# Kernel optimization log

Measured on AMD Instinct MI355X. Metric: run time of the kernel, lower is better.

Reference implementation:

```python
import jax, jax.numpy as jnp
import numpy as np
from jax import lax

N = 8388608
NG = 1024
TAU = 0.1
GAMMA = 0.05
MAX_ITERS = 30
EPS = 1e-9


def setup_inputs() -> dict:
    key = jax.random.key(0)
    k1, k2, k3 = jax.random.split(key, 3)
    y_raw = jax.random.uniform(k1, (N,), dtype=jnp.float32)
    y_real = jax.random.uniform(k2, (N,), dtype=jnp.float32)
    group_ids = jax.random.randint(k3, (N,), 0, NG, dtype=jnp.int32)
    return {"y_raw": y_raw, "y_real": y_real, "group_ids": group_ids, "n_groups": NG}


def reference(y_raw, y_real, group_ids, n_groups):
    y_real = jnp.maximum(y_real, EPS)
    l = (1.0 - TAU) * y_real          # per-element lower box bound
    u = (1.0 + TAU) * y_real          # per-element upper box bound
    y_clipped = jnp.clip(y_raw, l, u)
    w = 1.0 / jnp.maximum(y_real, 1e-9)

    seg_sum = lambda v: jax.ops.segment_sum(v, group_ids, num_segments=n_groups)

    n_g = seg_sum(jnp.ones_like(y_raw))            # [G] group sizes
    L = (1.0 - GAMMA) * n_g
    U = (1.0 + GAMMA) * n_g
    S0 = seg_sum(w * y_clipped)                    # [G] ratio sums at alpha=0
    feasible = (S0 >= L) & (S0 <= U)

    # per-group bracketing interval for alpha
    alo = jax.ops.segment_min((l - y_raw) * w, group_ids, num_segments=n_groups) - 1.0
    ahi = jax.ops.segment_max((u - y_raw) * w, group_ids, num_segments=n_groups) + 1.0
    nonempty = n_g > 0
    alo = jnp.where(nonempty, alo, 0.0)            # guard empty groups (inf/-inf)
    ahi = jnp.where(nonempty, ahi, 0.0)
    T = jnp.where(S0 < L, L, U)                    # [G] bisection target

    def step(carry, _):
        lo, hi, _ = carry
        mid = 0.5 * (lo + hi)                                    # [G]
        y_mid = jnp.clip(y_raw + mid[group_ids] / w, l, u)       # [N]
        Smid = seg_sum(w * y_mid)                                # [G]
        lo = jnp.where(Smid < T, mid, lo)
        hi = jnp.where(Smid >= T, mid, hi)
        return (lo, hi, mid), None

    (lo, hi, mid), _ = lax.scan(step, (alo, ahi, alo), None, length=MAX_ITERS)
    y_bis = jnp.clip(y_raw + mid[group_ids] / w, l, u)           # last iterate y_mid
    return jnp.where(feasible[group_ids], y_clipped, y_bis)
```

## Files before the change

### kernel.cpp

```cpp
#include <hip/hip_runtime.h>

#define NGROUPS  1024
#define EPSF     1e-9f
#define MAX_ITERS 30
#define SUM_MASK ((1ull << 49) - 1)
#define CNT_SHIFT 49
#define FIX_SCALE 1073741824.0f
#define FIX_INV   (1.0 / 1073741824.0)

__device__ __forceinline__ unsigned enc_f(float f) {
    unsigned u = __float_as_uint(f);
    return (u & 0x80000000u) ? ~u : (u | 0x80000000u);
}
__device__ __forceinline__ float dec_f(unsigned e) {
    unsigned u = (e & 0x80000000u) ? (e ^ 0x80000000u) : ~e;
    return __uint_as_float(u);
}

__global__ __launch_bounds__(NGROUPS) void k_init(unsigned long long* gpack,
                                                  unsigned* gmn, unsigned* gmx) {
    int g = threadIdx.x;
    gpack[g] = 0ull;
    gmn[g]   = 0xFFFFFFFFu;
    gmx[g]   = 0u;
}

__global__ __launch_bounds__(1024) void k_stats(const float4* __restrict__ yraw4,
                                                const float4* __restrict__ yreal4,
                                                const int4*   __restrict__ gid4,
                                                float4*       __restrict__ out4,
                                                unsigned long long* gpack, int n4) {
    __shared__ unsigned long long s_pk[NGROUPS];
    int t = threadIdx.x;
    s_pk[t] = 0ull;
    __syncthreads();

    int base = blockIdx.x * 4096;
    float4 yr[4], ye[4];
    int4   gg[4];
    bool   ok[4];
#pragma unroll
    for (int k = 0; k < 4; ++k) {
        int i = base + k * 1024 + t;
        ok[k] = (i < n4);
        if (ok[k]) { yr[k] = yraw4[i]; ye[k] = yreal4[i]; gg[k] = gid4[i]; }
    }
#pragma unroll
    for (int k = 0; k < 4; ++k) {
        if (!ok[k]) continue;
        float yrs[4] = { yr[k].x, yr[k].y, yr[k].z, yr[k].w };
        float yes[4] = { ye[k].x, ye[k].y, ye[k].z, ye[k].w };
        int   gs[4]  = { gg[k].x, gg[k].y, gg[k].z, gg[k].w };
        float oc[4];
#pragma unroll
        for (int j = 0; j < 4; ++j) {
            float yraw = yrs[j];
            float yrc  = fmaxf(yes[j], EPSF);
            float l = 0.9f * yrc;
            float u = 1.1f * yrc;
            float yclip = fminf(fmaxf(yraw, l), u);
            oc[j] = yclip;
            float s = yclip / yrc;
            unsigned long long pk = (1ull << CNT_SHIFT)
                + (unsigned long long)__float2uint_rn(s * FIX_SCALE);
            atomicAdd(&s_pk[gs[j]], pk);
        }
        out4[base + k * 1024 + t] = make_float4(oc[0], oc[1], oc[2], oc[3]);
    }
    __syncthreads();
    if (s_pk[t] != 0ull) atomicAdd(&gpack[t], s_pk[t]);
}

__global__ __launch_bounds__(NGROUPS) void k_group(const unsigned long long* gpack,
                                                   unsigned* feas, float* gT,
                                                   float* galpha, unsigned* gbase,
                                                   unsigned* gcur, unsigned* total) {
    __shared__ unsigned s_scan[NGROUPS];
    int g = threadIdx.x;
    unsigned long long pk = gpack[g];
    unsigned c = (unsigned)(pk >> CNT_SHIFT);
    float S0 = (float)((double)(pk & SUM_MASK) * FIX_INV);
    float n  = (float)c;
    float L = 0.95f * n;
    float U = 1.05f * n;
    unsigned f = (S0 >= L && S0 <= U) ? 1u : 0u;
    feas[g]   = f;
    gT[g]     = (S0 < L) ? L : U;
    galpha[g] = 0.0f;

    unsigned v = f ? 0u : c;
    s_scan[g] = v;
    for (int off = 1; off < NGROUPS; off <<= 1) {
        __syncthreads();
        unsigned tmp = (g >= off) ? s_scan[g - off] : 0u;
        __syncthreads();
        s_scan[g] += tmp;
    }
    __syncthreads();
    unsigned incl = s_scan[g];
    unsigned base = incl - v;
    gbase[g] = base;
    gcur[g]  = base;
    if (g == NGROUPS - 1) *total = incl;
}

__global__ __launch_bounds__(256) void k_mmc(const float4* __restrict__ yraw4,
                                             const float4* __restrict__ yreal4,
                                             const int4*   __restrict__ gid4,
                                             const unsigned* __restrict__ feas,
                                             unsigned* gcur, const unsigned* total,
                                             unsigned* gmn, unsigned* gmx,
                                             unsigned* cidx, unsigned* cgid,
                                             unsigned capacity, int n4) {
    if (*total == 0u) return;
    __shared__ unsigned s_feas[NGROUPS];
    __shared__ unsigned s_mn[NGROUPS];
    __shared__ unsigned s_mx[NGROUPS];
    for (int g = threadIdx.x; g < NGROUPS; g += blockDim.x) {
        s_feas[g] = feas[g]; s_mn[g] = 0xFFFFFFFFu; s_mx[g] = 0u;
    }
    __syncthreads();
    int stride = gridDim.x * blockDim.x;
    for (int i = blockIdx.x * blockDim.x + threadIdx.x; i < n4; i += stride) {
        int4 gg = gid4[i];
        int gs[4] = { gg.x, gg.y, gg.z, gg.w };
        bool any = !s_feas[gs[0]] || !s_feas[gs[1]] || !s_feas[gs[2]] || !s_feas[gs[3]];
        if (!any) continue;
        float4 yr = yraw4[i];
        float4 ye = yreal4[i];
        float yrs[4] = { yr.x, yr.y, yr.z, yr.w };
        float yes[4] = { ye.x, ye.y, ye.z, ye.w };
#pragma unroll
        for (int j = 0; j < 4; ++j) {
            int g = gs[j];
            if (s_feas[g]) continue;
            float yraw = yrs[j];
            float yrc  = fmaxf(yes[j], EPSF);
            float l = 0.9f * yrc;
            float u = 1.1f * yrc;
            float w = 1.0f / yrc;
            float a0 = (l - yraw) * w;
            float a1 = (u - yraw) * w;
            atomicMin(&s_mn[g], enc_f(a0));
            atomicMax(&s_mx[g], enc_f(a1));
            unsigned pos = atomicAdd(&gcur[g], 1u);
            if (pos < capacity) {
                cidx[pos] = (unsigned)(4 * i + j);
                cgid[pos] = (unsigned)g;
            }
        }
    }
    __syncthreads();
    for (int g = threadIdx.x; g < NGROUPS; g += blockDim.x) {
        if (!s_feas[g]) {
            atomicMin(&gmn[g], s_mn[g]);
            atomicMax(&gmx[g], s_mx[g]);
        }
    }
}

#define CAPC 8064
__global__ __launch_bounds__(256) void k_bisect(const float* __restrict__ y_raw,
                                                const float* __restrict__ y_real,
                                                const unsigned* feas,
                                                const unsigned long long* gpack,
                                                const unsigned* gbase, const float* gT,
                                                const unsigned* gmn, const unsigned* gmx,
                                                float* galpha,
                                                const unsigned* __restrict__ cidx,
                                                unsigned capacity) {
    int g = blockIdx.x;
    if (feas[g]) return;
    __shared__ float2 cache[CAPC];
    __shared__ double s_part[4];
    __shared__ float  s_mid;
    unsigned base = gbase[g];
    unsigned cnt  = (unsigned)(gpack[g] >> CNT_SHIFT);
    if (base >= capacity) cnt = 0;
    else if (cnt > capacity - base) cnt = capacity - base;
    int t = threadIdx.x;
    for (unsigned i = t; i < cnt && i < CAPC; i += 256u) {
        unsigned idx = cidx[base + i];
        cache[i] = make_float2(y_raw[idx], y_real[idx]);
    }
    __syncthreads();
    float lo = dec_f(gmn[g]) - 1.0f;
    float hi = dec_f(gmx[g]) + 1.0f;
    float T  = gT[g];
    float mid = lo;
    for (int it = 0; it < MAX_ITERS; ++it) {
        if (t == 0) s_mid = 0.5f * (lo + hi);
        __syncthreads();
        float m = s_mid;
        double part = 0.0;
        for (unsigned i = t; i < cnt; i += 256u) {
            float yraw, ye;
            if (i < CAPC) { float2 v = cache[i]; yraw = v.x; ye = v.y; }
            else { unsigned idx = cidx[base + i]; yraw = y_raw[idx]; ye = y_real[idx]; }
            float yrc = fmaxf(ye, EPSF);
            float l = 0.9f * yrc;
            float u = 1.1f * yrc;
            float w = 1.0f / yrc;
            float ym = fminf(fmaxf(yraw + m / w, l), u);
            part += (double)(w * ym);
        }
#pragma unroll
        for (int off = 32; off > 0; off >>= 1) part += __shfl_down(part, off, 64);
        if ((t & 63) == 0) s_part[t >> 6] = part;
        __syncthreads();
        if (t == 0) {
            float Smid = (float)(s_part[0] + s_part[1] + s_part[2] + s_part[3]);
            if (Smid < T) lo = m; else hi = m;
        }
        mid = m;
        __syncthreads();
    }
    if (t == 0) galpha[g] = mid;
}

__global__ __launch_bounds__(256) void k_fixup(const float* __restrict__ y_raw,
                                               const float* __restrict__ y_real,
                                               const unsigned* __restrict__ cidx,
                                               const unsigned* __restrict__ cgid,
                                               const float* galpha, const unsigned* total,
                                               float* __restrict__ out, unsigned capacity) {
    unsigned tot = *total;
    if (tot > capacity) tot = capacity;
    unsigned stride = gridDim.x * blockDim.x;
    for (unsigned i = blockIdx.x * blockDim.x + threadIdx.x; i < tot; i += stride) {
        unsigned idx = cidx[i];
        unsigned g   = cgid[i];
        float yraw = y_raw[idx];
        float yrc  = fmaxf(y_real[idx], EPSF);
        float l = 0.9f * yrc;
        float u = 1.1f * yrc;
        float w = 1.0f / yrc;
        float a = galpha[g];
        out[idx] = fminf(fmaxf(yraw + a / w, l), u);
    }
}

extern "C" void kernel_launch(void* const* d_in, const int* in_sizes, int n_in,
                              void* d_out, int out_size, void* d_ws, size_t ws_size,
                              hipStream_t stream) {
    const float* y_raw  = (const float*)d_in[0];
    const float* y_real = (const float*)d_in[1];
    const int*   gid    = (const int*)d_in[2];
    float* out = (float*)d_out;
    const int n  = in_sizes[0];
    const int n4 = n / 4;

    char* ws = (char*)d_ws;
    unsigned long long* gpack = (unsigned long long*)(ws + 0);
    unsigned* gmn    = (unsigned*)(ws + 8192);
    unsigned* gmx    = (unsigned*)(ws + 12288);
    unsigned* feas   = (unsigned*)(ws + 16384);
    float*    gT     = (float*)(ws + 20480);
    float*    galpha = (float*)(ws + 24576);
    unsigned* gbase  = (unsigned*)(ws + 28672);
    unsigned* gcur   = (unsigned*)(ws + 32768);
    unsigned* total  = (unsigned*)(ws + 36864);
    unsigned* cidx   = (unsigned*)(ws + 40960);
    size_t cap64 = (ws_size > 40960) ? (ws_size - 40960) / 8 : 0;
    if (cap64 > (size_t)n) cap64 = (size_t)n;
    unsigned capacity = (unsigned)cap64;
    unsigned* cgid = cidx + capacity;

    int nb_stats = (n4 + 4095) / 4096;

    k_init<<<1, NGROUPS, 0, stream>>>(gpack, gmn, gmx);
    k_stats<<<nb_stats, 1024, 0, stream>>>((const float4*)y_raw, (const float4*)y_real,
                                           (const int4*)gid, (float4*)out, gpack, n4);
    k_group<<<1, NGROUPS, 0, stream>>>(gpack, feas, gT, galpha, gbase, gcur, total);
    k_mmc<<<512, 256, 0, stream>>>((const float4*)y_raw, (const float4*)y_real,
                                   (const int4*)gid, feas, gcur, total,
                                   gmn, gmx, cidx, cgid, capacity, n4);
    k_bisect<<<NGROUPS, 256, 0, stream>>>(y_raw, y_real, feas, gpack, gbase, gT,
                                          gmn, gmx, galpha, cidx, capacity);
    k_fixup<<<512, 256, 0, stream>>>(y_raw, y_real, cidx, cgid, galpha, total,
                                     out, capacity);
}
```

Measured before the change: 150.7 us.

## Fuse group finalize into stats via last-block and fixup into bisection

Merges the per-group feasibility and prefix-scan kernel into the stats kernel, using a last-block-done counter with a threadfence. Bisection blocks now write the final clipped outputs for their own group, so the separate fixup kernel goes away. Stats switches to 512-thread blocks, adds an exact-tiling variant without bounds checks, and uses nontemporal output stores. The aim is to remove two launches and their serialization gaps, at the cost of a serial tail in the last block and a dependence on the done counter being reset each call.

Measured after the change: 410.3 us. +172.3%, slower.

```diff
diff --git a/kernel.cpp b/kernel.cpp
--- a/kernel.cpp
+++ b/kernel.cpp
@@ -7,6 +7,10 @@
 #define CNT_SHIFT 49
 #define FIX_SCALE 1073741824.0f
 #define FIX_INV   (1.0 / 1073741824.0)
+#define SBLK 512
+#define STILE 4
+
+typedef float vfloat4 __attribute__((ext_vector_type(4)));
 
 __device__ __forceinline__ unsigned enc_f(float f) {
     unsigned u = __float_as_uint(f);
@@ -18,90 +22,129 @@
 }
 
 __global__ __launch_bounds__(NGROUPS) void k_init(unsigned long long* gpack,
-                                                  unsigned* gmn, unsigned* gmx) {
+                                                  unsigned* done) {
     int g = threadIdx.x;
     gpack[g] = 0ull;
-    gmn[g]   = 0xFFFFFFFFu;
-    gmx[g]   = 0u;
-}
-
-__global__ __launch_bounds__(1024) void k_stats(const float4* __restrict__ yraw4,
+    if (g == 0) *done = 0u;
+}
+
+template <bool EXACT>
+__global__ __launch_bounds__(SBLK) void k_stats(const float4* __restrict__ yraw4,
                                                 const float4* __restrict__ yreal4,
                                                 const int4*   __restrict__ gid4,
                                                 float4*       __restrict__ out4,
-                                                unsigned long long* gpack, int n4) {
+                                                unsigned long long* gpack,
+                                                unsigned* done,
+                                                unsigned* feas, float* gT,
+                                                unsigned* gmn, unsigned* gmx,
+                                                unsigned* gbase, unsigned* gcur,
+                                                unsigned* total, int n4) {
     __shared__ unsigned long long s_pk[NGROUPS];
     int t = threadIdx.x;
-    s_pk[t] = 0ull;
-    __syncthreads();
-
-    int base = blockIdx.x * 4096;
-    float4 yr[4], ye[4];
-    int4   gg[4];
-    bool   ok[4];
-#pragma unroll
-    for (int k = 0; k < 4; ++k) {
-        int i = base + k * 1024 + t;
-        ok[k] = (i < n4);
-        if (ok[k]) { yr[k] = yraw4[i]; ye[k] = yreal4[i]; gg[k] = gid4[i]; }
-    }
-#pragma unroll
-    for (int k = 0; k < 4; ++k) {
-        if (!ok[k]) continue;
-        float yrs[4] = { yr[k].x, yr[k].y, yr[k].z, yr[k].w };
-        float yes[4] = { ye[k].x, ye[k].y, ye[k].z, ye[k].w };
-        int   gs[4]  = { gg[k].x, gg[k].y, gg[k].z, gg[k].w };
-        float oc[4];
-#pragma unroll
-        for (int j = 0; j < 4; ++j) {
-            float yraw = yrs[j];
-            float yrc  = fmaxf(yes[j], EPSF);
-            float l = 0.9f * yrc;
-            float u = 1.1f * yrc;
-            float yclip = fminf(fmaxf(yraw, l), u);
-            oc[j] = yclip;
-            float s = yclip / yrc;
-            unsigned long long pk = (1ull << CNT_SHIFT)
-                + (unsigned long long)__float2uint_rn(s * FIX_SCALE);
-            atomicAdd(&s_pk[gs[j]], pk);
-        }
-        out4[base + k * 1024 + t] = make_float4(oc[0], oc[1], oc[2], oc[3]);
-    }
-    __syncthreads();
-    if (s_pk[t] != 0ull) atomicAdd(&gpack[t], s_pk[t]);
-}
-
-__global__ __launch_bounds__(NGROUPS) void k_group(const unsigned long long* gpack,
-                                                   unsigned* feas, float* gT,
-                                                   float* galpha, unsigned* gbase,
-                                                   unsigned* gcur, unsigned* total) {
-    __shared__ unsigned s_scan[NGROUPS];
-    int g = threadIdx.x;
-    unsigned long long pk = gpack[g];
-    unsigned c = (unsigned)(pk >> CNT_SHIFT);
-    float S0 = (float)((double)(pk & SUM_MASK) * FIX_INV);
-    float n  = (float)c;
-    float L = 0.95f * n;
-    float U = 1.05f * n;
-    unsigned f = (S0 >= L && S0 <= U) ? 1u : 0u;
-    feas[g]   = f;
-    gT[g]     = (S0 < L) ? L : U;
-    galpha[g] = 0.0f;
-
-    unsigned v = f ? 0u : c;
-    s_scan[g] = v;
-    for (int off = 1; off < NGROUPS; off <<= 1) {
-        __syncthreads();
-        unsigned tmp = (g >= off) ? s_scan[g - off] : 0u;
-        __syncthreads();
-        s_scan[g] += tmp;
-    }
-    __syncthreads();
-    unsigned incl = s_scan[g];
-    unsigned base = incl - v;
-    gbase[g] = base;
-    gcur[g]  = base;
-    if (g == NGROUPS - 1) *total = incl;
+    s_pk[t] = 0ull; s_pk[t + SBLK] = 0ull;
+    __syncthreads();
+
+    int base = blockIdx.x * (SBLK * STILE) + t;
+    float4 yr[STILE], ye[STILE];
+    int4   gg[STILE];
+    if (EXACT) {
+#pragma unroll
+        for (int k = 0; k < STILE; ++k) yr[k] = yraw4[base + k * SBLK];
+#pragma unroll
+        for (int k = 0; k < STILE; ++k) ye[k] = yreal4[base + k * SBLK];
+#pragma unroll
+        for (int k = 0; k < STILE; ++k) gg[k] = gid4[base + k * SBLK];
+#pragma unroll
+        for (int k = 0; k < STILE; ++k) {
+            float yrs[4] = { yr[k].x, yr[k].y, yr[k].z, yr[k].w };
+            float yes[4] = { ye[k].x, ye[k].y, ye[k].z, ye[k].w };
+            int   gs[4]  = { gg[k].x, gg[k].y, gg[k].z, gg[k].w };
+            float oc[4];
+#pragma unroll
+            for (int j = 0; j < 4; ++j) {
+                float yraw = yrs[j];
+                float yrc  = fmaxf(yes[j], EPSF);
+                float l = 0.9f * yrc;
+                float u = 1.1f * yrc;
+                float yclip = fminf(fmaxf(yraw, l), u);
+                oc[j] = yclip;
+                float s = yclip / yrc;
+                unsigned long long pk = (1ull << CNT_SHIFT)
+                    + (unsigned long long)__float2uint_rn(s * FIX_SCALE);
+                atomicAdd(&s_pk[gs[j]], pk);
+            }
+            vfloat4 ov = { oc[0], oc[1], oc[2], oc[3] };
+            __builtin_nontemporal_store(ov, (vfloat4*)&out4[base + k * SBLK]);
+        }
+    } else {
+#pragma unroll
+        for (int k = 0; k < STILE; ++k) {
+            int i = base + k * SBLK;
+            if (i >= n4) continue;
+            float4 a = yraw4[i], b = yreal4[i];
+            int4 g4 = gid4[i];
+            float yrs[4] = { a.x, a.y, a.z, a.w };
+            float yes[4] = { b.x, b.y, b.z, b.w };
+            int   gs[4]  = { g4.x, g4.y, g4.z, g4.w };
+            float oc[4];
+#pragma unroll
+            for (int j = 0; j < 4; ++j) {
+                float yrc  = fmaxf(yes[j], EPSF);
+                float l = 0.9f * yrc, u = 1.1f * yrc;
+                float yclip = fminf(fmaxf(yrs[j], l), u);
+                oc[j] = yclip;
+                unsigned long long pk = (1ull << CNT_SHIFT)
+                    + (unsigned long long)__float2uint_rn((yclip / yrc) * FIX_SCALE);
+                atomicAdd(&s_pk[gs[j]], pk);
+            }
+            out4[i] = make_float4(oc[0], oc[1], oc[2], oc[3]);
+        }
+    }
+    __syncthreads();
+    {
+        unsigned long long v0 = s_pk[t], v1 = s_pk[t + SBLK];
+        if (v0) atomicAdd(&gpack[t], v0);
+        if (v1) atomicAdd(&gpack[t + SBLK], v1);
+    }
+    __shared__ int s_last;
+    __threadfence();
+    __syncthreads();
+    if (t == 0) s_last = (atomicAdd(done, 1u) == gridDim.x - 1) ? 1 : 0;
+    __syncthreads();
+    if (!s_last) return;
+
+    __shared__ unsigned s_v[NGROUPS];
+    __shared__ unsigned s_ps[SBLK];
+    for (int g = t; g < NGROUPS; g += SBLK) {
+        unsigned long long pk = atomicAdd(&gpack[g], 0ull);
+        unsigned c = (unsigned)(pk >> CNT_SHIFT);
+        float S0 = (float)((double)(pk & SUM_MASK) * FIX_INV);
+        float nf = (float)c;
+        float L = 0.95f * nf;
+        float U = 1.05f * nf;
+        unsigned f = (S0 >= L && S0 <= U) ? 1u : 0u;
+        feas[g] = f;
+        gT[g]   = (S0 < L) ? L : U;
+        gmn[g]  = 0xFFFFFFFFu;
+        gmx[g]  = 0u;
+        s_v[g]  = f ? 0u : c;
+    }
+    __syncthreads();
+    unsigned a0 = s_v[2 * t], a1 = s_v[2 * t + 1];
+    unsigned ps = a0 + a1;
+    s_ps[t] = ps;
+    for (int off = 1; off < SBLK; off <<= 1) {
+        __syncthreads();
+        unsigned tmp = (t >= off) ? s_ps[t - off] : 0u;
+        __syncthreads();
+        s_ps[t] += tmp;
+    }
+    __syncthreads();
+    unsigned incl = s_ps[t];
+    unsigned b0 = incl - ps;
+    gbase[2 * t]     = b0;      gcur[2 * t]     = b0;
+    gbase[2 * t + 1] = b0 + a0; gcur[2 * t + 1] = b0 + a0;
+    if (t == SBLK - 1) *total = incl;
 }
 
 __global__ __launch_bounds__(256) void k_mmc(const float4* __restrict__ yraw4,
@@ -166,8 +209,8 @@
                                                 const unsigned long long* gpack,
                                                 const unsigned* gbase, const float* gT,
                                                 const unsigned* gmn, const unsigned* gmx,
-                                                float* galpha,
                                                 const unsigned* __restrict__ cidx,
+                                                float* __restrict__ out,
                                                 unsigned capacity) {
     int g = blockIdx.x;
     if (feas[g]) return;
@@ -187,7 +230,6 @@
     float lo = dec_f(gmn[g]) - 1.0f;
     float hi = dec_f(gmx[g]) + 1.0f;
     float T  = gT[g];
-    float mid = lo;
     for (int it = 0; it < MAX_ITERS; ++it) {
         if (t == 0) s_mid = 0.5f * (lo + hi);
         __syncthreads();
@@ -212,31 +254,19 @@
             float Smid = (float)(s_part[0] + s_part[1] + s_part[2] + s_part[3]);
             if (Smid < T) lo = m; else hi = m;
         }
-        mid = m;
-        __syncthreads();
-    }
-    if (t == 0) galpha[g] = mid;
-}
-
-__global__ __launch_bounds__(256) void k_fixup(const float* __restrict__ y_raw,
-                                               const float* __restrict__ y_real,
-                                               const unsigned* __restrict__ cidx,
-                                               const unsigned* __restrict__ cgid,
-                                               const float* galpha, const unsigned* total,
-                                               float* __restrict__ out, unsigned capacity) {
-    unsigned tot = *total;
-    if (tot > capacity) tot = capacity;
-    unsigned stride = gridDim.x * blockDim.x;
-    for (unsigned i = blockIdx.x * blockDim.x + threadIdx.x; i < tot; i += stride) {
-        unsigned idx = cidx[i];
-        unsigned g   = cgid[i];
-        float yraw = y_raw[idx];
-        float yrc  = fmaxf(y_real[idx], EPSF);
+        __syncthreads();
+    }
+    float m = s_mid;
+    for (unsigned i = t; i < cnt; i += 256u) {
+        unsigned idx = cidx[base + i];
+        float yraw, ye;
+        if (i < CAPC) { float2 v = cache[i]; yraw = v.x; ye = v.y; }
+        else { yraw = y_raw[idx]; ye = y_real[idx]; }
+        float yrc = fmaxf(ye, EPSF);
         float l = 0.9f * yrc;
         float u = 1.1f * yrc;
         float w = 1.0f / yrc;
-        float a = galpha[g];
-        out[idx] = fminf(fmaxf(yraw + a / w, l), u);
+        out[idx] = fminf(fmaxf(yraw + m / w, l), u);
     }
 }
 
@@ -256,27 +286,30 @@
     unsigned* gmx    = (unsigned*)(ws + 12288);
     unsigned* feas   = (unsigned*)(ws + 16384);
     float*    gT     = (float*)(ws + 20480);
-    float*    galpha = (float*)(ws + 24576);
-    unsigned* gbase  = (unsigned*)(ws + 28672);
-    unsigned* gcur   = (unsigned*)(ws + 32768);
-    unsigned* total  = (unsigned*)(ws + 36864);
+    unsigned* gbase  = (unsigned*)(ws + 24576);
+    unsigned* gcur   = (unsigned*)(ws + 28672);
+    unsigned* total  = (unsigned*)(ws + 32768);
+    unsigned* done   = (unsigned*)(ws + 36864);
     unsigned* cidx   = (unsigned*)(ws + 40960);
     size_t cap64 = (ws_size > 40960) ? (ws_size - 40960) / 8 : 0;
     if (cap64 > (size_t)n) cap64 = (size_t)n;
     unsigned capacity = (unsigned)cap64;
     unsigned* cgid = cidx + capacity;
 
-    int nb_stats = (n4 + 4095) / 4096;
-
-    k_init<<<1, NGROUPS, 0, stream>>>(gpack, gmn, gmx);
-    k_stats<<<nb_stats, 1024, 0, stream>>>((const float4*)y_raw, (const float4*)y_real,
-                                           (const int4*)gid, (float4*)out, gpack, n4);
-    k_group<<<1, NGROUPS, 0, stream>>>(gpack, feas, gT, galpha, gbase, gcur, total);
+    const int per_blk = SBLK * STILE;
+    k_init<<<1, NGROUPS, 0, stream>>>(gpack, done);
+    if (n4 % per_blk == 0) {
+        k_stats<true><<<n4 / per_blk, SBLK, 0, stream>>>(
+            (const float4*)y_raw, (const float4*)y_real, (const int4*)gid,
+            (float4*)out, gpack, done, feas, gT, gmn, gmx, gbase, gcur, total, n4);
+    } else {
+        k_stats<false><<<(n4 + per_blk - 1) / per_blk, SBLK, 0, stream>>>(
+            (const float4*)y_raw, (const float4*)y_real, (const int4*)gid,
+            (float4*)out, gpack, done, feas, gT, gmn, gmx, gbase, gcur, total, n4);
+    }
     k_mmc<<<512, 256, 0, stream>>>((const float4*)y_raw, (const float4*)y_real,
                                    (const int4*)gid, feas, gcur, total,
                                    gmn, gmx, cidx, cgid, capacity, n4);
     k_bisect<<<NGROUPS, 256, 0, stream>>>(y_raw, y_real, feas, gpack, gbase, gT,
-                                          gmn, gmx, galpha, cidx, capacity);
-    k_fixup<<<512, 256, 0, stream>>>(y_raw, y_real, cidx, cgid, galpha, total,
-                                     out, capacity);
-}
+                                          gmn, gmx, cidx, out, capacity);
+}
```
